# Kernel tuning notes

Hardware: AMD Instinct MI355X
Metric: run time of the kernel (lower is better)

## Reference

```python
import jax, jax.numpy as jnp
import numpy as np

E = 1024   # embedding_dim (d_model)
F = 4096   # hidden_dim (dim_feedforward)
N = 64     # num_documents
L = 2      # encoder layers
H = 8      # nhead
LN_EPS = 1e-5


def _layer_norm(x, g, b):
    m = jnp.mean(x, axis=-1, keepdims=True)
    v = jnp.mean((x - m) ** 2, axis=-1, keepdims=True)  # biased var, like torch LN
    return (x - m) / jnp.sqrt(v + LN_EPS) * g + b


def setup_inputs() -> dict:
    key = jax.random.key(0)
    ks = iter(jax.random.split(key, 40))
    s = 0.02
    d = {
        "query_emb": jax.random.normal(next(ks), (E,), jnp.float32),
        "doc_embs": jax.random.normal(next(ks), (N, E), jnp.float32),
        # query_doc_projector: Linear(2E -> E)
        "proj_W": jax.random.normal(next(ks), (2 * E, E), jnp.float32) * s,
        "proj_b": jnp.zeros((E,), jnp.float32),
        # 2 TransformerEncoderLayers (post-norm, relu), stacked on leading dim L
        "Wqkv": jax.random.normal(next(ks), (L, E, 3 * E), jnp.float32) * s,
        "bqkv": jnp.zeros((L, 3 * E), jnp.float32),
        "Wo": jax.random.normal(next(ks), (L, E, E), jnp.float32) * s,
        "bo": jnp.zeros((L, E), jnp.float32),
        "ln1_g": jnp.ones((L, E), jnp.float32),
        "ln1_b": jnp.zeros((L, E), jnp.float32),
        "ln2_g": jnp.ones((L, E), jnp.float32),
        "ln2_b": jnp.zeros((L, E), jnp.float32),
        "W1": jax.random.normal(next(ks), (L, E, F), jnp.float32) * s,
        "b1": jnp.zeros((L, F), jnp.float32),
        "W2": jax.random.normal(next(ks), (L, F, E), jnp.float32) * s,
        "b2": jnp.zeros((L, E), jnp.float32),
        # attention_score MLP: E -> F -> 1
        "Wa1": jax.random.normal(next(ks), (E, F), jnp.float32) * s,
        "ba1": jnp.zeros((F,), jnp.float32),
        "Wa2": jax.random.normal(next(ks), (F, 1), jnp.float32) * s,
        "ba2": jnp.zeros((1,), jnp.float32),
        # fusion MLP: E -> F -> F
        "Wf1": jax.random.normal(next(ks), (E, F), jnp.float32) * s,
        "bf1": jnp.zeros((F,), jnp.float32),
        "Wf2": jax.random.normal(next(ks), (F, F), jnp.float32) * s,
        "bf2": jnp.zeros((F,), jnp.float32),
    }
    return d


def reference(query_emb, doc_embs, proj_W, proj_b, Wqkv, bqkv, Wo, bo,
              ln1_g, ln1_b, ln2_g, ln2_b, W1, b1, W2, b2,
              Wa1, ba1, Wa2, ba2, Wf1, bf1, Wf2, bf2):
    n = doc_embs.shape[0]
    # [query, doc] concat per document, batched across all docs: [N, 2E]
    ctx = jnp.concatenate([jnp.broadcast_to(query_emb, doc_embs.shape), doc_embs], axis=-1)
    x = ctx @ proj_W + proj_b  # [N, E]
    # TransformerEncoder with seq_len=1 per document (eval mode, dropout off).
    # Self-attention over a single token: softmax of one score == 1, so the
    # attention output is exactly out_proj(v) (identical value AND gradient).
    for l in range(L):
        qkv = x @ Wqkv[l] + bqkv[l]                 # [N, 3E]
        v = qkv[:, 2 * E:]                          # [N, E]
        attn = v @ Wo[l] + bo[l]                    # [N, E]
        x = _layer_norm(x + attn, ln1_g[l], ln1_b[l])
        h = jax.nn.relu(x @ W1[l] + b1[l]) @ W2[l] + b2[l]
        x = _layer_norm(x + h, ln2_g[l], ln2_b[l])
    # attention over documents
    logits = jax.nn.relu(x @ Wa1 + ba1) @ Wa2 + ba2   # [N, 1]
    w = jax.nn.softmax(logits, axis=0)                # softmax over docs
    fused = jnp.sum(x * w, axis=0)                    # [E]
    fused_repr = jax.nn.relu(fused @ Wf1 + bf1) @ Wf2 + bf2  # [F]
    return fused_repr[None, :], w.squeeze(-1)
```

## Files before the change

kernel.cpp:

```cpp
#include <hip/hip_runtime.h>
#include <math.h>


#define EDIM 1024
#define FDIM 4096

__device__ __forceinline__ float block_sum256(float v) {
  __shared__ float lds[4];
  #pragma unroll
  for (int off = 32; off; off >>= 1) v += __shfl_down(v, off);
  const int wid  = threadIdx.x >> 6;
  const int lane = threadIdx.x & 63;
  __syncthreads();
  if (lane == 0) lds[wid] = v;
  __syncthreads();
  return lds[0] + lds[1] + lds[2] + lds[3];
}

#define FMA4(ACC, S, W4) \
  ACC.x = fmaf(S, W4.x, ACC.x); ACC.y = fmaf(S, W4.y, ACC.y); \
  ACC.z = fmaf(S, W4.z, ACC.z); ACC.w = fmaf(S, W4.w, ACC.w);

template<int MODE_A>
__global__ __launch_bounds__(256)
void gemm64_k(const float* __restrict__ A, int lda,
              const float* __restrict__ qv, const float* __restrict__ doc,
              const float* __restrict__ W, int ldw,
              float* __restrict__ P, int Nout, int Kt)
{
  __shared__ float As[64 * 68];
  __shared__ float Ws[64 * 68];
  const int t  = threadIdx.x;
  const int cg = t & 15;
  const int rg = t >> 4;
  const int r0 = rg * 4;
  const int jb = blockIdx.x * 64;
  const int jc = jb + cg * 4;
  const int kb = blockIdx.y * Kt;

  float4 acc[4];
  #pragma unroll
  for (int i = 0; i < 4; ++i) acc[i] = make_float4(0.f, 0.f, 0.f, 0.f);

  for (int k0 = kb; k0 < kb + Kt; k0 += 64) {
    __syncthreads();
    #pragma unroll
    for (int it = 0; it < 4; ++it) {
      const int p   = t + it * 256;
      const int row = p >> 4;
      const int c4  = (p & 15) * 4;
      const int k   = k0 + c4;
      float4 val;
      if (MODE_A == 1)
        val = (k < EDIM) ? *(const float4*)(qv + k)
                         : *(const float4*)(doc + (size_t)row * EDIM + (k - EDIM));
      else
        val = *(const float4*)(A + (size_t)row * lda + k);
      *(float4*)(As + row * 68 + c4) = val;
    }
    #pragma unroll
    for (int it = 0; it < 4; ++it) {
      const int p   = t + it * 256;
      const int row = p >> 4;
      const int c4  = (p & 15) * 4;
      const float4 val = *(const float4*)(W + (size_t)(k0 + row) * ldw + jb + c4);
      *(float4*)(Ws + row * 68 + c4) = val;
    }
    __syncthreads();
    #pragma unroll 4
    for (int kk4 = 0; kk4 < 64; kk4 += 4) {
      const float4 a0 = *(const float4*)(As + (r0 + 0) * 68 + kk4);
      const float4 a1 = *(const float4*)(As + (r0 + 1) * 68 + kk4);
      const float4 a2 = *(const float4*)(As + (r0 + 2) * 68 + kk4);
      const float4 a3 = *(const float4*)(As + (r0 + 3) * 68 + kk4);
      const float4 w0 = *(const float4*)(Ws + (kk4 + 0) * 68 + cg * 4);
      const float4 w1 = *(const float4*)(Ws + (kk4 + 1) * 68 + cg * 4);
      const float4 w2 = *(const float4*)(Ws + (kk4 + 2) * 68 + cg * 4);
      const float4 w3 = *(const float4*)(Ws + (kk4 + 3) * 68 + cg * 4);
      FMA4(acc[0], a0.x, w0) FMA4(acc[0], a0.y, w1) FMA4(acc[0], a0.z, w2) FMA4(acc[0], a0.w, w3)
      FMA4(acc[1], a1.x, w0) FMA4(acc[1], a1.y, w1) FMA4(acc[1], a1.z, w2) FMA4(acc[1], a1.w, w3)
      FMA4(acc[2], a2.x, w0) FMA4(acc[2], a2.y, w1) FMA4(acc[2], a2.z, w2) FMA4(acc[2], a2.w, w3)
      FMA4(acc[3], a3.x, w0) FMA4(acc[3], a3.y, w1) FMA4(acc[3], a3.z, w2) FMA4(acc[3], a3.w, w3)
    }
  }

  float* o = P + (size_t)blockIdx.y * 64 * Nout;
  #pragma unroll
  for (int i = 0; i < 4; ++i)
    *(float4*)(o + (size_t)(r0 + i) * Nout + jc) = acc[i];
}

template<int LN, int HAS_RES>
__global__ __launch_bounds__(256)
void reduce_row_k(const float* __restrict__ P, int S,
                  const float* __restrict__ bias,
                  const float* __restrict__ res,
                  const float* __restrict__ g, const float* __restrict__ bln,
                  float* __restrict__ out)
{
  const int row = blockIdx.x;
  const int c   = threadIdx.x * 4;
  float4 v = make_float4(0.f, 0.f, 0.f, 0.f);
  for (int s = 0; s < S; ++s) {
    const float4 p = *(const float4*)(P + ((size_t)s * 64 + row) * EDIM + c);
    v.x += p.x; v.y += p.y; v.z += p.z; v.w += p.w;
  }
  const float4 b4 = *(const float4*)(bias + c);
  v.x += b4.x; v.y += b4.y; v.z += b4.z; v.w += b4.w;
  if (HAS_RES) {
    const float4 r4 = *(const float4*)(res + (size_t)row * EDIM + c);
    v.x += r4.x; v.y += r4.y; v.z += r4.z; v.w += r4.w;
  }
  if (LN) {
    float mean = block_sum256(v.x + v.y + v.z + v.w) * (1.f / 1024.f);
    float dx = v.x - mean, dy = v.y - mean, dz = v.z - mean, dw = v.w - mean;
    float var  = block_sum256(dx * dx + dy * dy + dz * dz + dw * dw) * (1.f / 1024.f);
    float inv  = 1.f / sqrtf(var + 1e-5f);
    const float4 g4  = *(const float4*)(g + c);
    const float4 bl4 = *(const float4*)(bln + c);
    v.x = dx * inv * g4.x + bl4.x;
    v.y = dy * inv * g4.y + bl4.y;
    v.z = dz * inv * g4.z + bl4.z;
    v.w = dw * inv * g4.w + bl4.w;
  }
  *(float4*)(out + (size_t)row * EDIM + c) = v;
}

template<int RELU>
__global__ __launch_bounds__(256)
void reduce_wide_k(const float* __restrict__ P, int S,
                   const float* __restrict__ bias, float* __restrict__ out)
{
  const int j4   = blockIdx.x * 256 + threadIdx.x;
  const int flat = j4 * 4;
  const int col  = flat & (FDIM - 1);
  float4 v = make_float4(0.f, 0.f, 0.f, 0.f);
  for (int s = 0; s < S; ++s) {
    const float4 p = *(const float4*)(P + (size_t)s * 64 * FDIM + flat);
    v.x += p.x; v.y += p.y; v.z += p.z; v.w += p.w;
  }
  const float4 b4 = *(const float4*)(bias + col);
  v.x += b4.x; v.y += b4.y; v.z += b4.z; v.w += b4.w;
  if (RELU) { v.x = fmaxf(v.x, 0.f); v.y = fmaxf(v.y, 0.f);
              v.z = fmaxf(v.z, 0.f); v.w = fmaxf(v.w, 0.f); }
  *(float4*)(out + flat) = v;
}

__global__ __launch_bounds__(256)
void logits_k(const float* __restrict__ a, const float* __restrict__ Wa2,
              const float* __restrict__ ba2, float* __restrict__ logits)
{
  const int i = blockIdx.x;
  const float* ar = a + (size_t)i * FDIM;
  float v = 0.f;
  for (int cidx = threadIdx.x; cidx < FDIM; cidx += 256)
    v = fmaf(ar[cidx], Wa2[cidx], v);
  float s = block_sum256(v);
  if (threadIdx.x == 0) logits[i] = s + ba2[0];
}

__global__ __launch_bounds__(256)
void pool_k(const float* __restrict__ logits, const float* __restrict__ x,
            float* __restrict__ fused, float* __restrict__ w_out)
{
  __shared__ float l[64];
  __shared__ float wl[64];
  const int t = threadIdx.x;
  if (t < 64) l[t] = logits[t];
  __syncthreads();
  float m = -1e30f;
  for (int i = 0; i < 64; ++i) m = fmaxf(m, l[i]);
  float den = 0.f;
  for (int i = 0; i < 64; ++i) den += expf(l[i] - m);
  if (t < 64) wl[t] = expf(l[t] - m) / den;
  __syncthreads();
  const int j = blockIdx.x * 256 + t;
  float acc = 0.f;
  for (int i = 0; i < 64; ++i) acc = fmaf(wl[i], x[(size_t)i * EDIM + j], acc);
  fused[j] = acc;
  if (blockIdx.x == 0 && t < 64) w_out[t] = wl[t];
}

template<int KT>
__global__ __launch_bounds__(256)
void gemv_k(const float* __restrict__ vec, const float* __restrict__ W, int Ncol,
            float* __restrict__ P)
{
  __shared__ float vl[KT];
  const int t  = threadIdx.x;
  const int k0 = blockIdx.y * KT;
  for (int k = t; k < KT; k += 256) vl[k] = vec[k0 + k];
  __syncthreads();
  const int j = blockIdx.x * 1024 + t * 4;
  const float* wp = W + (size_t)k0 * Ncol + j;
  float4 acc = make_float4(0.f, 0.f, 0.f, 0.f);
  #pragma unroll 8
  for (int kk = 0; kk < KT; ++kk) {
    const float4 w = *(const float4*)(wp + (size_t)kk * Ncol);
    const float s = vl[kk];
    acc.x = fmaf(s, w.x, acc.x); acc.y = fmaf(s, w.y, acc.y);
    acc.z = fmaf(s, w.z, acc.z); acc.w = fmaf(s, w.w, acc.w);
  }
  *(float4*)(P + (size_t)blockIdx.y * Ncol + j) = acc;
}

template<int RELU>
__global__ __launch_bounds__(256)
void reduce_vec_k(const float* __restrict__ P, int S, int Ncol,
                  const float* __restrict__ bias, float* __restrict__ out)
{
  const int j = blockIdx.x * 256 + threadIdx.x;
  float v = 0.f;
  for (int s = 0; s < S; ++s) v += P[(size_t)s * Ncol + j];
  v += bias[j];
  if (RELU) v = fmaxf(v, 0.f);
  out[j] = v;
}

extern "C" void kernel_launch(void* const* d_in, const int* in_sizes, int n_in,
                              void* d_out, int out_size, void* d_ws, size_t ws_size,
                              hipStream_t stream) {
  (void)in_sizes; (void)n_in; (void)out_size; (void)ws_size;
  const float* q    = (const float*)d_in[0];
  const float* doc  = (const float*)d_in[1];
  const float* Wp   = (const float*)d_in[2];
  const float* bp   = (const float*)d_in[3];
  const float* Wqkv = (const float*)d_in[4];
  const float* bqkv = (const float*)d_in[5];
  const float* Wo   = (const float*)d_in[6];
  const float* bo   = (const float*)d_in[7];
  const float* ln1g = (const float*)d_in[8];
  const float* ln1b = (const float*)d_in[9];
  const float* ln2g = (const float*)d_in[10];
  const float* ln2b = (const float*)d_in[11];
  const float* W1   = (const float*)d_in[12];
  const float* b1   = (const float*)d_in[13];
  const float* W2   = (const float*)d_in[14];
  const float* b2   = (const float*)d_in[15];
  const float* Wa1  = (const float*)d_in[16];
  const float* ba1  = (const float*)d_in[17];
  const float* Wa2  = (const float*)d_in[18];
  const float* ba2  = (const float*)d_in[19];
  const float* Wf1  = (const float*)d_in[20];
  const float* bf1  = (const float*)d_in[21];
  const float* Wf2  = (const float*)d_in[22];
  const float* bf2  = (const float*)d_in[23];
  float* out = (float*)d_out;
  float* ws  = (float*)d_ws;

  float* x      = ws;
  float* v      = ws + 65536;
  float* h      = ws + 131072;
  float* a      = ws + 393216;
  float* P      = ws + 655360;
  float* Pw     = P;
  float* logits = ws + 2752512;
  float* fused  = ws + 2752576;
  float* g      = ws + 2753600;
  float* Pf     = P;
  float* P2     = P + 262144;

  const dim3 blk(256);

  gemm64_k<1><<<dim3(16,16), blk, 0, stream>>>(nullptr, 0, q, doc, Wp, EDIM, P, EDIM, 128);
  reduce_row_k<0,0><<<64, blk, 0, stream>>>(P, 16, bp, nullptr, nullptr, nullptr, x);

  for (int l = 0; l < 2; ++l) {
    const float* Wv = Wqkv + (size_t)l * EDIM * 3 * EDIM + 2 * EDIM;
    gemm64_k<0><<<dim3(16,16), blk, 0, stream>>>(x, EDIM, nullptr, nullptr, Wv, 3 * EDIM, P, EDIM, 64);
    reduce_row_k<0,0><<<64, blk, 0, stream>>>(P, 16, bqkv + l * 3 * EDIM + 2 * EDIM, nullptr, nullptr, nullptr, v);

    gemm64_k<0><<<dim3(16,16), blk, 0, stream>>>(v, EDIM, nullptr, nullptr, Wo + (size_t)l * EDIM * EDIM, EDIM, P, EDIM, 64);
    reduce_row_k<1,1><<<64, blk, 0, stream>>>(P, 16, bo + l * EDIM, x, ln1g + l * EDIM, ln1b + l * EDIM, x);

    gemm64_k<0><<<dim3(64,8), blk, 0, stream>>>(x, EDIM, nullptr, nullptr, W1 + (size_t)l * EDIM * FDIM, FDIM, Pw, FDIM, 128);
    reduce_wide_k<1><<<256, blk, 0, stream>>>(Pw, 8, b1 + l * FDIM, h);

    gemm64_k<0><<<dim3(16,32), blk, 0, stream>>>(h, FDIM, nullptr, nullptr, W2 + (size_t)l * FDIM * EDIM, EDIM, P, EDIM, 128);
    reduce_row_k<1,1><<<64, blk, 0, stream>>>(P, 32, b2 + l * EDIM, x, ln2g + l * EDIM, ln2b + l * EDIM, x);
  }

  gemm64_k<0><<<dim3(64,8), blk, 0, stream>>>(x, EDIM, nullptr, nullptr, Wa1, FDIM, Pw, FDIM, 128);
  reduce_wide_k<1><<<256, blk, 0, stream>>>(Pw, 8, ba1, a);
  logits_k<<<64, blk, 0, stream>>>(a, Wa2, ba2, logits);
  pool_k<<<4, blk, 0, stream>>>(logits, x, fused, out + FDIM);

  gemv_k<16><<<dim3(4,64), blk, 0, stream>>>(fused, Wf1, FDIM, Pf);
  reduce_vec_k<1><<<16, blk, 0, stream>>>(Pf, 64, FDIM, bf1, g);
  gemv_k<64><<<dim3(4,64), blk, 0, stream>>>(g, Wf2, FDIM, P2);
  reduce_vec_k<0><<<16, blk, 0, stream>>>(P2, 64, FDIM, bf2, out);
}
```

Before: 230.8 us.

## Replace split-K partial buffers with fixed-point 64-bit atomic accumulation and fused epilogues

Each GEMM and GEMV now accumulates its split-K partials directly into zero-initialised int64 fixed-point buffers with atomicAdd, which removes the separate reduction kernels. Bias, ReLU and the residual are applied when the next GEMM loads its A tile or inside the layer-norm and logits kernels. The aim is to cut kernel launches and the round trips through global memory for partial buffers. In exchange it adds a large memset, a high volume of 64-bit atomics with double conversions, and rounding from the fixed-point scale that makes results order-independent but slightly less precise.

```diff
diff --git a/kernel.cpp b/kernel.cpp
--- a/kernel.cpp
+++ b/kernel.cpp
@@ -4,6 +4,18 @@
 
 #define EDIM 1024
 #define FDIM 4096
+
+typedef long long ll;
+typedef unsigned long long ull;
+#define SCALE_D  1099511627776.0
+#define INV_SCALE 9.094947017729282e-13
+
+__device__ __forceinline__ float i2f(ll v) {
+  return (float)((double)v * INV_SCALE);
+}
+__device__ __forceinline__ void atomg(ull* p, float v) {
+  atomicAdd(p, (ull)__double2ll_rn((double)v * SCALE_D));
+}
 
 __device__ __forceinline__ float block_sum256(float v) {
   __shared__ float lds[4];
@@ -23,20 +35,21 @@
 
 template<int MODE_A>
 __global__ __launch_bounds__(256)
-void gemm64_k(const float* __restrict__ A, int lda,
-              const float* __restrict__ qv, const float* __restrict__ doc,
-              const float* __restrict__ W, int ldw,
-              float* __restrict__ P, int Nout, int Kt)
+void gemm_k(const float* __restrict__ Af, int lda_f,
+            const ll* __restrict__ Ai, int lda_i,
+            const float* __restrict__ abias,
+            const float* __restrict__ qv, const float* __restrict__ doc,
+            const float* __restrict__ W, int ldw,
+            ull* __restrict__ Acc, int Nout, int Kt)
 {
   __shared__ float As[64 * 68];
   __shared__ float Ws[64 * 68];
-  const int t  = threadIdx.x;
-  const int cg = t & 15;
-  const int rg = t >> 4;
-  const int r0 = rg * 4;
-  const int jb = blockIdx.x * 64;
-  const int jc = jb + cg * 4;
-  const int kb = blockIdx.y * Kt;
+  const int t   = threadIdx.x;
+  const int cgi = t & 15;
+  const int r0  = (t >> 4) * 4;
+  const int jb  = blockIdx.x * 64;
+  const int jc  = jb + cgi * 4;
+  const int kb  = blockIdx.y * Kt;
 
   float4 acc[4];
   #pragma unroll
@@ -46,25 +59,35 @@
     __syncthreads();
     #pragma unroll
     for (int it = 0; it < 4; ++it) {
-      const int p   = t + it * 256;
-      const int row = p >> 4;
-      const int c4  = (p & 15) * 4;
+      const int pi  = t + it * 256;
+      const int row = pi >> 4;
+      const int c4  = (pi & 15) * 4;
       const int k   = k0 + c4;
       float4 val;
-      if (MODE_A == 1)
+      if (MODE_A == 0) {
+        val = *(const float4*)(Af + (size_t)row * lda_f + k);
+      } else if (MODE_A == 1) {
         val = (k < EDIM) ? *(const float4*)(qv + k)
                          : *(const float4*)(doc + (size_t)row * EDIM + (k - EDIM));
-      else
-        val = *(const float4*)(A + (size_t)row * lda + k);
+      } else {
+        const ll* ap = Ai + (size_t)row * lda_i + k;
+        const float4 b4 = *(const float4*)(abias + k);
+        val.x = i2f(ap[0]) + b4.x; val.y = i2f(ap[1]) + b4.y;
+        val.z = i2f(ap[2]) + b4.z; val.w = i2f(ap[3]) + b4.w;
+        if (MODE_A == 3) {
+          val.x = fmaxf(val.x, 0.f); val.y = fmaxf(val.y, 0.f);
+          val.z = fmaxf(val.z, 0.f); val.w = fmaxf(val.w, 0.f);
+        }
+      }
       *(float4*)(As + row * 68 + c4) = val;
     }
     #pragma unroll
     for (int it = 0; it < 4; ++it) {
-      const int p   = t + it * 256;
-      const int row = p >> 4;
-      const int c4  = (p & 15) * 4;
-      const float4 val = *(const float4*)(W + (size_t)(k0 + row) * ldw + jb + c4);
-      *(float4*)(Ws + row * 68 + c4) = val;
+      const int pi  = t + it * 256;
+      const int row = pi >> 4;
+      const int c4  = (pi & 15) * 4;
+      *(float4*)(Ws + row * 68 + c4) =
+          *(const float4*)(W + (size_t)(k0 + row) * ldw + jb + c4);
     }
     __syncthreads();
     #pragma unroll 4
@@ -73,106 +96,97 @@
       const float4 a1 = *(const float4*)(As + (r0 + 1) * 68 + kk4);
       const float4 a2 = *(const float4*)(As + (r0 + 2) * 68 + kk4);
       const float4 a3 = *(const float4*)(As + (r0 + 3) * 68 + kk4);
-      const float4 w0 = *(const float4*)(Ws + (kk4 + 0) * 68 + cg * 4);
-      const float4 w1 = *(const float4*)(Ws + (kk4 + 1) * 68 + cg * 4);
-      const float4 w2 = *(const float4*)(Ws + (kk4 + 2) * 68 + cg * 4);
-      const float4 w3 = *(const float4*)(Ws + (kk4 + 3) * 68 + cg * 4);
+      const float4 w0 = *(const float4*)(Ws + (kk4 + 0) * 68 + cgi * 4);
+      const float4 w1 = *(const float4*)(Ws + (kk4 + 1) * 68 + cgi * 4);
+      const float4 w2 = *(const float4*)(Ws + (kk4 + 2) * 68 + cgi * 4);
+      const float4 w3 = *(const float4*)(Ws + (kk4 + 3) * 68 + cgi * 4);
       FMA4(acc[0], a0.x, w0) FMA4(acc[0], a0.y, w1) FMA4(acc[0], a0.z, w2) FMA4(acc[0], a0.w, w3)
       FMA4(acc[1], a1.x, w0) FMA4(acc[1], a1.y, w1) FMA4(acc[1], a1.z, w2) FMA4(acc[1], a1.w, w3)
       FMA4(acc[2], a2.x, w0) FMA4(acc[2], a2.y, w1) FMA4(acc[2], a2.z, w2) FMA4(acc[2], a2.w, w3)
       FMA4(acc[3], a3.x, w0) FMA4(acc[3], a3.y, w1) FMA4(acc[3], a3.z, w2) FMA4(acc[3], a3.w, w3)
     }
   }
-
-  float* o = P + (size_t)blockIdx.y * 64 * Nout;
-  #pragma unroll
-  for (int i = 0; i < 4; ++i)
-    *(float4*)(o + (size_t)(r0 + i) * Nout + jc) = acc[i];
-}
-
-template<int LN, int HAS_RES>
-__global__ __launch_bounds__(256)
-void reduce_row_k(const float* __restrict__ P, int S,
-                  const float* __restrict__ bias,
-                  const float* __restrict__ res,
-                  const float* __restrict__ g, const float* __restrict__ bln,
-                  float* __restrict__ out)
+  #pragma unroll
+  for (int i = 0; i < 4; ++i) {
+    ull* d = Acc + (size_t)(r0 + i) * Nout + jc;
+    atomg(d + 0, acc[i].x); atomg(d + 1, acc[i].y);
+    atomg(d + 2, acc[i].z); atomg(d + 3, acc[i].w);
+  }
+}
+
+template<int RESI>
+__global__ __launch_bounds__(256)
+void ln_k(const ll* __restrict__ acc, const float* __restrict__ bias,
+          const float* __restrict__ resf,
+          const ll* __restrict__ resi, const float* __restrict__ rbias,
+          const float* __restrict__ gam, const float* __restrict__ bet,
+          float* __restrict__ outp)
 {
   const int row = blockIdx.x;
   const int c   = threadIdx.x * 4;
-  float4 v = make_float4(0.f, 0.f, 0.f, 0.f);
-  for (int s = 0; s < S; ++s) {
-    const float4 p = *(const float4*)(P + ((size_t)s * 64 + row) * EDIM + c);
-    v.x += p.x; v.y += p.y; v.z += p.z; v.w += p.w;
-  }
+  const ll* ap = acc + (size_t)row * EDIM + c;
   const float4 b4 = *(const float4*)(bias + c);
-  v.x += b4.x; v.y += b4.y; v.z += b4.z; v.w += b4.w;
-  if (HAS_RES) {
-    const float4 r4 = *(const float4*)(res + (size_t)row * EDIM + c);
+  float4 v;
+  v.x = i2f(ap[0]) + b4.x; v.y = i2f(ap[1]) + b4.y;
+  v.z = i2f(ap[2]) + b4.z; v.w = i2f(ap[3]) + b4.w;
+  if (RESI) {
+    const ll* rp = resi + (size_t)row * EDIM + c;
+    const float4 rb = *(const float4*)(rbias + c);
+    v.x += i2f(rp[0]) + rb.x; v.y += i2f(rp[1]) + rb.y;
+    v.z += i2f(rp[2]) + rb.z; v.w += i2f(rp[3]) + rb.w;
+  } else {
+    const float4 r4 = *(const float4*)(resf + (size_t)row * EDIM + c);
     v.x += r4.x; v.y += r4.y; v.z += r4.z; v.w += r4.w;
   }
-  if (LN) {
-    float mean = block_sum256(v.x + v.y + v.z + v.w) * (1.f / 1024.f);
-    float dx = v.x - mean, dy = v.y - mean, dz = v.z - mean, dw = v.w - mean;
-    float var  = block_sum256(dx * dx + dy * dy + dz * dz + dw * dw) * (1.f / 1024.f);
-    float inv  = 1.f / sqrtf(var + 1e-5f);
-    const float4 g4  = *(const float4*)(g + c);
-    const float4 bl4 = *(const float4*)(bln + c);
-    v.x = dx * inv * g4.x + bl4.x;
-    v.y = dy * inv * g4.y + bl4.y;
-    v.z = dz * inv * g4.z + bl4.z;
-    v.w = dw * inv * g4.w + bl4.w;
-  }
-  *(float4*)(out + (size_t)row * EDIM + c) = v;
-}
-
-template<int RELU>
-__global__ __launch_bounds__(256)
-void reduce_wide_k(const float* __restrict__ P, int S,
-                   const float* __restrict__ bias, float* __restrict__ out)
-{
-  const int j4   = blockIdx.x * 256 + threadIdx.x;
-  const int flat = j4 * 4;
-  const int col  = flat & (FDIM - 1);
-  float4 v = make_float4(0.f, 0.f, 0.f, 0.f);
-  for (int s = 0; s < S; ++s) {
-    const float4 p = *(const float4*)(P + (size_t)s * 64 * FDIM + flat);
-    v.x += p.x; v.y += p.y; v.z += p.z; v.w += p.w;
-  }
-  const float4 b4 = *(const float4*)(bias + col);
-  v.x += b4.x; v.y += b4.y; v.z += b4.z; v.w += b4.w;
-  if (RELU) { v.x = fmaxf(v.x, 0.f); v.y = fmaxf(v.y, 0.f);
-              v.z = fmaxf(v.z, 0.f); v.w = fmaxf(v.w, 0.f); }
-  *(float4*)(out + flat) = v;
-}
-
-__global__ __launch_bounds__(256)
-void logits_k(const float* __restrict__ a, const float* __restrict__ Wa2,
-              const float* __restrict__ ba2, float* __restrict__ logits)
-{
-  const int i = blockIdx.x;
-  const float* ar = a + (size_t)i * FDIM;
-  float v = 0.f;
-  for (int cidx = threadIdx.x; cidx < FDIM; cidx += 256)
-    v = fmaf(ar[cidx], Wa2[cidx], v);
-  float s = block_sum256(v);
-  if (threadIdx.x == 0) logits[i] = s + ba2[0];
+  const float mean = block_sum256(v.x + v.y + v.z + v.w) * (1.f / 1024.f);
+  const float dx = v.x - mean, dy = v.y - mean, dz = v.z - mean, dw = v.w - mean;
+  const float var = block_sum256(dx * dx + dy * dy + dz * dz + dw * dw) * (1.f / 1024.f);
+  const float inv = 1.f / sqrtf(var + 1e-5f);
+  const float4 g4 = *(const float4*)(gam + c);
+  const float4 l4 = *(const float4*)(bet + c);
+  float4 o;
+  o.x = dx * inv * g4.x + l4.x; o.y = dy * inv * g4.y + l4.y;
+  o.z = dz * inv * g4.z + l4.z; o.w = dw * inv * g4.w + l4.w;
+  *(float4*)(outp + (size_t)row * EDIM + c) = o;
+}
+
+__global__ __launch_bounds__(256)
+void logits_k(const ll* __restrict__ wa1acc, const float* __restrict__ ba1,
+              const float* __restrict__ Wa2, const float* __restrict__ ba2,
+              float* __restrict__ logits)
+{
+  const int row = blockIdx.x;
+  const int t   = threadIdx.x;
+  float dot = 0.f;
+  #pragma unroll
+  for (int i = 0; i < 4; ++i) {
+    const int col = (t + i * 256) * 4;
+    const ll* ap = wa1acc + (size_t)row * FDIM + col;
+    const float4 b4 = *(const float4*)(ba1 + col);
+    float4 v;
+    v.x = fmaxf(i2f(ap[0]) + b4.x, 0.f); v.y = fmaxf(i2f(ap[1]) + b4.y, 0.f);
+    v.z = fmaxf(i2f(ap[2]) + b4.z, 0.f); v.w = fmaxf(i2f(ap[3]) + b4.w, 0.f);
+    const float4 w2 = *(const float4*)(Wa2 + col);
+    dot = fmaf(v.x, w2.x, fmaf(v.y, w2.y, fmaf(v.z, w2.z, fmaf(v.w, w2.w, dot))));
+  }
+  const float s = block_sum256(dot);
+  if (t == 0) logits[row] = s + ba2[0];
 }
 
 __global__ __launch_bounds__(256)
 void pool_k(const float* __restrict__ logits, const float* __restrict__ x,
             float* __restrict__ fused, float* __restrict__ w_out)
 {
-  __shared__ float l[64];
+  __shared__ float llv[64];
   __shared__ float wl[64];
   const int t = threadIdx.x;
-  if (t < 64) l[t] = logits[t];
+  if (t < 64) llv[t] = logits[t];
   __syncthreads();
   float m = -1e30f;
-  for (int i = 0; i < 64; ++i) m = fmaxf(m, l[i]);
+  for (int i = 0; i < 64; ++i) m = fmaxf(m, llv[i]);
   float den = 0.f;
-  for (int i = 0; i < 64; ++i) den += expf(l[i] - m);
-  if (t < 64) wl[t] = expf(l[t] - m) / den;
+  for (int i = 0; i < 64; ++i) den += expf(llv[i] - m);
+  if (t < 64) wl[t] = expf(llv[t] - m) / den;
   __syncthreads();
   const int j = blockIdx.x * 256 + t;
   float acc = 0.f;
@@ -181,40 +195,46 @@
   if (blockIdx.x == 0 && t < 64) w_out[t] = wl[t];
 }
 
-template<int KT>
-__global__ __launch_bounds__(256)
-void gemv_k(const float* __restrict__ vec, const float* __restrict__ W, int Ncol,
-            float* __restrict__ P)
-{
-  __shared__ float vl[KT];
+__global__ __launch_bounds__(256)
+void gemv1_k(const float* __restrict__ fused, const float* __restrict__ Wf1,
+             ull* __restrict__ gacc)
+{
+  __shared__ float vl[32];
   const int t  = threadIdx.x;
-  const int k0 = blockIdx.y * KT;
-  for (int k = t; k < KT; k += 256) vl[k] = vec[k0 + k];
-  __syncthreads();
-  const int j = blockIdx.x * 1024 + t * 4;
-  const float* wp = W + (size_t)k0 * Ncol + j;
-  float4 acc = make_float4(0.f, 0.f, 0.f, 0.f);
-  #pragma unroll 8
-  for (int kk = 0; kk < KT; ++kk) {
-    const float4 w = *(const float4*)(wp + (size_t)kk * Ncol);
-    const float s = vl[kk];
-    acc.x = fmaf(s, w.x, acc.x); acc.y = fmaf(s, w.y, acc.y);
-    acc.z = fmaf(s, w.z, acc.z); acc.w = fmaf(s, w.w, acc.w);
-  }
-  *(float4*)(P + (size_t)blockIdx.y * Ncol + j) = acc;
-}
-
-template<int RELU>
-__global__ __launch_bounds__(256)
-void reduce_vec_k(const float* __restrict__ P, int S, int Ncol,
-                  const float* __restrict__ bias, float* __restrict__ out)
+  const int k0 = blockIdx.y * 32;
+  if (t < 32) vl[t] = fused[k0 + t];
+  __syncthreads();
+  const int col = blockIdx.x * 256 + t;
+  const float* wp = Wf1 + (size_t)k0 * FDIM + col;
+  float acc = 0.f;
+  #pragma unroll
+  for (int kk = 0; kk < 32; ++kk) acc = fmaf(vl[kk], wp[(size_t)kk * FDIM], acc);
+  atomg(gacc + col, acc);
+}
+
+__global__ __launch_bounds__(256)
+void gemv2_k(const ll* __restrict__ gacc, const float* __restrict__ bf1,
+             const float* __restrict__ Wf2, ull* __restrict__ f2acc)
+{
+  __shared__ float vl[128];
+  const int t  = threadIdx.x;
+  const int k0 = blockIdx.y * 128;
+  if (t < 128) vl[t] = fmaxf(i2f(gacc[k0 + t]) + bf1[k0 + t], 0.f);
+  __syncthreads();
+  const int col = blockIdx.x * 256 + t;
+  const float* wp = Wf2 + (size_t)k0 * FDIM + col;
+  float acc = 0.f;
+  #pragma unroll 16
+  for (int kk = 0; kk < 128; ++kk) acc = fmaf(vl[kk], wp[(size_t)kk * FDIM], acc);
+  atomg(f2acc + col, acc);
+}
+
+__global__ __launch_bounds__(256)
+void final_k(const ll* __restrict__ f2acc, const float* __restrict__ bf2,
+             float* __restrict__ out)
 {
   const int j = blockIdx.x * 256 + threadIdx.x;
-  float v = 0.f;
-  for (int s = 0; s < S; ++s) v += P[(size_t)s * Ncol + j];
-  v += bias[j];
-  if (RELU) v = fmaxf(v, 0.f);
-  out[j] = v;
+  out[j] = i2f(f2acc[j]) + bf2[j];
 }
 
 extern "C" void kernel_launch(void* const* d_in, const int* in_sizes, int n_in,
@@ -246,47 +266,74 @@
   const float* Wf2  = (const float*)d_in[22];
   const float* bf2  = (const float*)d_in[23];
   float* out = (float*)d_out;
-  float* ws  = (float*)d_ws;
-
-  float* x      = ws;
-  float* v      = ws + 65536;
-  float* h      = ws + 131072;
-  float* a      = ws + 393216;
-  float* P      = ws + 655360;
-  float* Pw     = P;
-  float* logits = ws + 2752512;
-  float* fused  = ws + 2752576;
-  float* g      = ws + 2753600;
-  float* Pf     = P;
-  float* P2     = P + 262144;
+
+  ll*  ab = (ll*)d_ws;
+  ll* projacc = ab;
+  ll* vacc    = ab + 65536;
+  ll* attnacc = ab + 196608;
+  ll* ffn1acc = ab + 327680;
+  ll* ffn2acc = ab + 851968;
+  ll* wa1acc  = ab + 983040;
+  ll* gacc    = ab + 1245184;
+  ll* f2acc   = ab + 1249280;
+  const size_t accll = 1253376;
+  float* fb    = (float*)(ab + accll);
+  float* xbuf  = fb;
+  float* fused = fb + 65536;
+  float* logit = fb + 66560;
 
   const dim3 blk(256);
 
-  gemm64_k<1><<<dim3(16,16), blk, 0, stream>>>(nullptr, 0, q, doc, Wp, EDIM, P, EDIM, 128);
-  reduce_row_k<0,0><<<64, blk, 0, stream>>>(P, 16, bp, nullptr, nullptr, nullptr, x);
+  (void)hipMemsetAsync(ab, 0, accll * 8, stream);
+
+  gemm_k<1><<<dim3(16,32), blk, 0, stream>>>(nullptr, 0, nullptr, 0, nullptr,
+      q, doc, Wp, EDIM, (ull*)projacc, EDIM, 64);
 
   for (int l = 0; l < 2; ++l) {
-    const float* Wv = Wqkv + (size_t)l * EDIM * 3 * EDIM + 2 * EDIM;
-    gemm64_k<0><<<dim3(16,16), blk, 0, stream>>>(x, EDIM, nullptr, nullptr, Wv, 3 * EDIM, P, EDIM, 64);
-    reduce_row_k<0,0><<<64, blk, 0, stream>>>(P, 16, bqkv + l * 3 * EDIM + 2 * EDIM, nullptr, nullptr, nullptr, v);
-
-    gemm64_k<0><<<dim3(16,16), blk, 0, stream>>>(v, EDIM, nullptr, nullptr, Wo + (size_t)l * EDIM * EDIM, EDIM, P, EDIM, 64);
-    reduce_row_k<1,1><<<64, blk, 0, stream>>>(P, 16, bo + l * EDIM, x, ln1g + l * EDIM, ln1b + l * EDIM, x);
-
-    gemm64_k<0><<<dim3(64,8), blk, 0, stream>>>(x, EDIM, nullptr, nullptr, W1 + (size_t)l * EDIM * FDIM, FDIM, Pw, FDIM, 128);
-    reduce_wide_k<1><<<256, blk, 0, stream>>>(Pw, 8, b1 + l * FDIM, h);
-
-    gemm64_k<0><<<dim3(16,32), blk, 0, stream>>>(h, FDIM, nullptr, nullptr, W2 + (size_t)l * FDIM * EDIM, EDIM, P, EDIM, 128);
-    reduce_row_k<1,1><<<64, blk, 0, stream>>>(P, 32, b2 + l * EDIM, x, ln2g + l * EDIM, ln2b + l * EDIM, x);
-  }
-
-  gemm64_k<0><<<dim3(64,8), blk, 0, stream>>>(x, EDIM, nullptr, nullptr, Wa1, FDIM, Pw, FDIM, 128);
-  reduce_wide_k<1><<<256, blk, 0, stream>>>(Pw, 8, ba1, a);
-  logits_k<<<64, blk, 0, stream>>>(a, Wa2, ba2, logits);
-  pool_k<<<4, blk, 0, stream>>>(logits, x, fused, out + FDIM);
-
-  gemv_k<16><<<dim3(4,64), blk, 0, stream>>>(fused, Wf1, FDIM, Pf);
-  reduce_vec_k<1><<<16, blk, 0, stream>>>(Pf, 64, FDIM, bf1, g);
-  gemv_k<64><<<dim3(4,64), blk, 0, stream>>>(g, Wf2, FDIM, P2);
-  reduce_vec_k<0><<<16, blk, 0, stream>>>(P2, 64, FDIM, bf2, out);
-}
+    const float* Wv  = Wqkv + (size_t)l * EDIM * 3 * EDIM + 2 * EDIM;
+    const float* bv  = bqkv + l * 3 * EDIM + 2 * EDIM;
+    const float* Wol = Wo + (size_t)l * EDIM * EDIM;
+    const float* W1l = W1 + (size_t)l * EDIM * FDIM;
+    const float* W2l = W2 + (size_t)l * FDIM * EDIM;
+    ll* vacc_l    = vacc    + (size_t)l * 65536;
+    ll* attnacc_l = attnacc + (size_t)l * 65536;
+    ll* ffn1acc_l = ffn1acc + (size_t)l * 262144;
+    ll* ffn2acc_l = ffn2acc + (size_t)l * 65536;
+
+    if (l == 0)
+      gemm_k<2><<<dim3(16,16), blk, 0, stream>>>(nullptr, 0, projacc, EDIM, bp,
+          nullptr, nullptr, Wv, 3 * EDIM, (ull*)vacc_l, EDIM, 64);
+    else
+      gemm_k<0><<<dim3(16,16), blk, 0, stream>>>(xbuf, EDIM, nullptr, 0, nullptr,
+          nullptr, nullptr, Wv, 3 * EDIM, (ull*)vacc_l, EDIM, 64);
+
+    gemm_k<2><<<dim3(16,16), blk, 0, stream>>>(nullptr, 0, vacc_l, EDIM, bv,
+        nullptr, nullptr, Wol, EDIM, (ull*)attnacc_l, EDIM, 64);
+
+    if (l == 0)
+      ln_k<1><<<64, blk, 0, stream>>>(attnacc_l, bo + l * EDIM, nullptr,
+          projacc, bp, ln1g + l * EDIM, ln1b + l * EDIM, xbuf);
+    else
+      ln_k<0><<<64, blk, 0, stream>>>(attnacc_l, bo + l * EDIM, xbuf,
+          nullptr, nullptr, ln1g + l * EDIM, ln1b + l * EDIM, xbuf);
+
+    gemm_k<0><<<dim3(64,8), blk, 0, stream>>>(xbuf, EDIM, nullptr, 0, nullptr,
+        nullptr, nullptr, W1l, FDIM, (ull*)ffn1acc_l, FDIM, 128);
+
+    gemm_k<3><<<dim3(16,32), blk, 0, stream>>>(nullptr, 0, ffn1acc_l, FDIM,
+        b1 + (size_t)l * FDIM, nullptr, nullptr, W2l, EDIM, (ull*)ffn2acc_l, EDIM, 128);
+
+    ln_k<0><<<64, blk, 0, stream>>>(ffn2acc_l, b2 + l * EDIM, xbuf,
+        nullptr, nullptr, ln2g + l * EDIM, ln2b + l * EDIM, xbuf);
+  }
+
+  gemm_k<0><<<dim3(64,8), blk, 0, stream>>>(xbuf, EDIM, nullptr, 0, nullptr,
+      nullptr, nullptr, Wa1, FDIM, (ull*)wa1acc, FDIM, 128);
+
+  logits_k<<<64, blk, 0, stream>>>(wa1acc, ba1, Wa2, ba2, logit);
+  pool_k<<<4, blk, 0, stream>>>(logit, xbuf, fused, out + FDIM);
+
+  gemv1_k<<<dim3(16,32), blk, 0, stream>>>(fused, Wf1, (ull*)gacc);
+  gemv2_k<<<dim3(16,32), blk, 0, stream>>>(gacc, bf1, Wf2, (ull*)f2acc);
+  final_k<<<16, blk, 0, stream>>>(f2acc, bf2, out);
+}
```

New measurement: 617.8 us. +167.7%, slower.
